# Optimization experiments

Hardware: AMD Instinct MI355X
Metric: run time of the kernel (lower is better)

The kernel has to match this reference:

```python
import jax, jax.numpy as jnp
import numpy as np
import math

B, S, D = 2048, 128, 64          # batch, seq_length, input_dim
H1, H2, OUT = 128, 128, 1        # sa_hidden, ta_hidden, output_dim


def _uniform(key, shape, stdv):
    return jax.random.uniform(key, shape, jnp.float32, -stdv, stdv)


def setup_inputs() -> dict:
    key = jax.random.key(0)
    ks = jax.random.split(key, 20)
    s1 = 1.0 / math.sqrt(H1)
    s2 = 1.0 / math.sqrt(H2)
    inp = {
        "X": jax.random.normal(ks[0], (B, S, D), jnp.float32),
        # SpatialLSTM params (stdv = 1/sqrt(sa_hidden))
        "sa_W": _uniform(ks[1], (D, 4 * H1), s1),
        "sa_U": _uniform(ks[2], (H1, 4 * H1), s1),
        "sa_b": _uniform(ks[3], (4 * H1,), s1),
        "sa_Wa": _uniform(ks[4], (D, D), s1),
        "sa_Ua": _uniform(ks[5], (2 * H1, D), s1),
        "sa_ba": _uniform(ks[6], (D,), s1),
        "sa_Va": _uniform(ks[7], (D, D), s1),
        # TemporalLSTM params (stdv = 1/sqrt(ta_hidden))
        "ta_Wa": _uniform(ks[8], (H1, S), s2),
        "ta_Ua": _uniform(ks[9], (H2, S), s2),
        "ta_ba": _uniform(ks[10], (S,), s2),
        "ta_Va": _uniform(ks[11], (S, S), s2),
        "ta_W": _uniform(ks[12], (H1, 4 * H2), s2),
        "ta_U": _uniform(ks[13], (H2, 4 * H2), s2),
        "ta_b": _uniform(ks[14], (4 * H2,), s2),
        "ta_Wy": _uniform(ks[15], (OUT, 4 * H2), s2),
        "fc_w": _uniform(ks[16], (OUT, H2), s2),
        "fc_b": _uniform(ks[17], (OUT,), s2),
    }
    return inp


def _sta_forward(X, sa_W, sa_U, sa_b, sa_Wa, sa_Ua, sa_ba, sa_Va,
                 ta_Wa, ta_Ua, ta_ba, ta_Va, ta_W, ta_U, ta_b, ta_Wy,
                 fc_w, fc_b):
    x = X[:, :, :D]                       # [B,S,D]
    y0 = X[:, 0, D - 1:].reshape(-1, OUT)  # y[:,0,:] -> [B,OUT]
    batch = x.shape[0]

    # ---- SpatialLSTM: scan over time ----
    def sa_step(carry, x_t):
        h, c = carry
        a = jnp.tanh(x_t @ sa_Wa + jnp.concatenate([h, c], axis=1) @ sa_Ua + sa_ba) @ sa_Va
        alpha = jax.nn.softmax(a, axis=1)            # [B,D]
        xw = alpha * x_t
        gates = xw @ sa_W + h @ sa_U + sa_b          # [B,4H1]
        i = jax.nn.sigmoid(gates[:, :H1])
        f = jax.nn.sigmoid(gates[:, H1:2 * H1])
        g = jnp.tanh(gates[:, 2 * H1:3 * H1])
        o = jax.nn.sigmoid(gates[:, 3 * H1:])
        c = f * c + i * g
        h = o * jnp.tanh(c)
        return (h, c), (h, alpha)

    h0 = jnp.zeros((batch, H1), X.dtype)
    c0 = jnp.zeros((batch, H1), X.dtype)
    _, (hs, alphas) = jax.lax.scan(sa_step, (h0, c0), jnp.swapaxes(x, 0, 1))
    H = jnp.swapaxes(hs, 0, 1)  # [B,S,H1]

    # ---- TemporalLSTM: scan over time, attending over the full H ----
    # note: s_t in the original stays zero for all t, so its s_t @ Ua term is 0.
    def ta_step(carry, h_t):
        lh, lc, y_prev = carry
        beta = jax.nn.softmax(jnp.tanh(h_t @ ta_Wa + ta_ba) @ ta_Va, axis=1)  # [B,S]
        h_att = jnp.einsum('bs,bsd->bd', beta, H)     # weighted sum over time
        gates = h_att @ ta_W + lh @ ta_U + y_prev @ ta_Wy + ta_b
        i = jax.nn.sigmoid(gates[:, :H2])
        f = jax.nn.sigmoid(gates[:, H2:2 * H2])
        g = jnp.tanh(gates[:, 2 * H2:3 * H2])
        o = jax.nn.sigmoid(gates[:, 3 * H2:])
        lc = f * lc + i * g
        lh = o * jnp.tanh(lc)
        y = lh @ fc_w.T + fc_b
        return (lh, lc, y), beta

    lh0 = jnp.zeros((batch, H2), X.dtype)
    lc0 = jnp.zeros((batch, H2), X.dtype)
    (_, _, y_pred), betas = jax.lax.scan(ta_step, (lh0, lc0, y0), jnp.swapaxes(H, 0, 1))
    return y_pred, alphas, betas  # alphas: [S,B,D], betas: [S,B,S]


def reference(X, sa_W, sa_U, sa_b, sa_Wa, sa_Ua, sa_ba, sa_Va,
              ta_Wa, ta_Ua, ta_ba, ta_Va, ta_W, ta_U, ta_b, ta_Wy,
              fc_w, fc_b):
    return _sta_forward(X, sa_W, sa_U, sa_b, sa_Wa, sa_Ua, sa_ba, sa_Va,
                        ta_Wa, ta_Ua, ta_ba, ta_Va, ta_W, ta_U, ta_b, ta_Wy,
                        fc_w, fc_b)
```

## Files before the change

kernel.cpp:

```cpp
#include <hip/hip_runtime.h>


#define BB 2048
#define SS 128
#define DD 64
#define HH 128
#define NG 512
#define M  8
#define NT 512

#define A_OFF    ((size_t)BB)
#define BETA_OFF ((size_t)BB + (size_t)SS*BB*DD)
#define H_BYTES  ((size_t)BB*SS*HH*4)
#define G0_BYTES ((size_t)BB*SS*NG*4)

#define B1G_ELEMS (192*512)
#define B1A_ELEMS (320*64)
#define BVA_ELEMS (64*64)
#define B3_ELEMS  (256*512)
#define BW_ELEMS  (128*128)
#define GH_OFF 0
#define GL_OFF (B1G_ELEMS)
#define AH_OFF (2*B1G_ELEMS)
#define AL_OFF (2*B1G_ELEMS + B1A_ELEMS)
// ... 27 lines not shown
__device__ __forceinline__ float wmax64(float v){
#pragma unroll
  for (int m = 32; m; m >>= 1) v = fmaxf(v, __shfl_xor(v, m, 64));
  return v;
}
__device__ __forceinline__ float wsum64(float v){
#pragma unroll
  for (int m = 32; m; m >>= 1) v += __shfl_xor(v, m, 64);
  return v;
}

__global__ __launch_bounds__(256) void repack_kernel(
    const float* __restrict__ saW, const float* __restrict__ saU,
    const float* __restrict__ saWa, const float* __restrict__ saUa,
    const float* __restrict__ saVa,
    const float* __restrict__ taU, const float* __restrict__ taW,
    const float* __restrict__ taWa, const float* __restrict__ taVa,
    unsigned short* __restrict__ F)
{
  int id = blockIdx.x*256 + threadIdx.x;
  if (id < B1G_ELEMS){
    int k = id >> 9, n = id & 511;
    float v = (k < 128) ? saU[(size_t)k*NG + n] : saW[(size_t)(k-128)*NG + n];
    int kk = k >> 5, kw = k & 31, nt = n >> 4, nc = n & 15;
    int lane = ((kw >> 3) << 4) | nc, j = kw & 7;
    size_t off = ((size_t)(nt*6 + kk)*64 + lane)*8 + j;
    unsigned short hi = bf16rne(v);
    F[GH_OFF + off] = hi; F[GL_OFF + off] = bf16rne(v - bfval(hi));
  }
  if (id < B1A_ELEMS){
    int k = id >> 6, n = id & 63;
    float v = (k < 256) ? saUa[(size_t)k*DD + n] : saWa[(size_t)(k-256)*DD + n];
    int kt = k >> 5, kw = k & 31, nt = n >> 4, nc = n & 15;
    int lane = ((kw >> 3) << 4) | nc, j = kw & 7;
    size_t off = ((size_t)(nt*10 + kt)*64 + lane)*8 + j;
    unsigned short hi = bf16rne(v);
    F[AH_OFF + off] = hi; F[AL_OFF + off] = bf16rne(v - bfval(hi));
  }
  if (id < BVA_ELEMS){
    int k = id >> 6, n = id & 63;
    float v = saVa[(size_t)k*DD + n];
    int kt = k >> 5, kw = k & 31, nt = n >> 4, nc = n & 15;
    int lane = ((kw >> 3) << 4) | nc, j = kw & 7;
    size_t off = ((size_t)(nt*2 + kt)*64 + lane)*8 + j;
    unsigned short hi = bf16rne(v);
    F[VH_OFF + off] = hi; F[VL_OFF + off] = bf16rne(v - bfval(hi));
  }
  if (id < B3_ELEMS){
    int k = id >> 9, n = id & 511;
    float v = (k < HH) ? taU[(size_t)k*NG + n] : taW[(size_t)(k-HH)*NG + n];
    int kt = k >> 5, kw = k & 31, nt = n >> 4, nc = n & 15;
    int lane = ((kw >> 3) << 4) | nc, j = kw & 7;
    size_t off = ((size_t)(nt*8 + kt)*64 + lane)*8 + j;
    unsigned short hi = bf16rne(v);
    F[B3H_OFF + off] = hi; F[B3L_OFF + off] = bf16rne(v - bfval(hi));
  }
  if (id < BW_ELEMS){
    int k = id >> 7, n = id & 127;
    int kt = k >> 5, kw = k & 31, nt = n >> 4, nc = n & 15;
    int lane = ((kw >> 3) << 4) | nc, j = kw & 7;
    size_t off = ((size_t)(nt*4 + kt)*64 + lane)*8 + j;
    F[RW_OFF + off] = bf16rne(taWa[(size_t)k*SS + n]);
    F[RV_OFF + off] = bf16rne(taVa[(size_t)k*SS + n]);
  }
}

struct P1 {
  uint4 afh[12*64];
  uint4 afl[12*64];
  uint4 aah[2*64];
  uint4 aal[2*64];
  uint4 awh[2560];
  uint4 awl[2560];
  uint4 vh[512];
  uint4 vl[512];
  float xx[M][DD];
  float cc[M][HH];
  float red[2][M][64];
  float g[M][NG];
  float sbias[NG];
};
struct P2S { float A[32][HH]; float tmp[32][SS]; float bp[32][SS]; };

__global__ __launch_bounds__(NT, 2) __attribute__((amdgpu_waves_per_eu(2, 2)))
void mf_ph1_kernel(
    const float* __restrict__ X,   const float* __restrict__ sab,
    const float* __restrict__ saba,
    const unsigned short* __restrict__ Fr,
    float* __restrict__ out, float* __restrict__ Hws)
{
  __shared__ P1 sm;
  const int tid = threadIdx.x;
  const int b0  = blockIdx.x * M;
  const int w   = tid >> 6, l = tid & 63;

  {
    uint4 z4 = make_uint4(0,0,0,0);
    for (int i = tid; i < 12*64; i += NT){ sm.afh[i] = z4; sm.afl[i] = z4; }
    if (tid < 2*64){ sm.aah[tid] = z4; sm.aal[tid] = z4; }
    for (int i = tid; i < M*HH; i += NT) ((float*)sm.cc)[i] = 0.f;
    sm.sbias[tid] = sab[tid];
    const uint4* sh = (const uint4*)(Fr + AH_OFF);
    const uint4* sl = (const uint4*)(Fr + AL_OFF);
    for (int i = tid; i < 2560; i += NT){ sm.awh[i] = sh[i]; sm.awl[i] = sl[i]; }
    sm.vh[tid] = ((const uint4*)(Fr + VH_OFF))[tid];
    sm.vl[tid] = ((const uint4*)(Fr + VL_OFF))[tid];
  }
  __syncthreads();
  if (tid < 128){
    int r = tid >> 4, d0 = (tid & 15)*4;
    float4 v = *(const float4*)(X + (size_t)(b0+r)*SS*DD + d0);
    *(float4*)&sm.xx[r][d0] = v;
    unsigned short* AFH = (unsigned short*)sm.afh;
    unsigned short* AFL = (unsigned short*)sm.afl;
    int kt = 8 + (d0 >> 5), lane = (((d0 & 31) >> 3) << 4) | r, jj0 = d0 & 7;
    float vv[4] = {v.x, v.y, v.z, v.w};
#pragma unroll
    for (int p = 0; p < 4; ++p){
      unsigned short h_ = bf16rne(vv[p]);
      AFH[(kt*64 + lane)*8 + jj0 + p] = h_;
      AFL[(kt*64 + lane)*8 + jj0 + p] = bf16rne(vv[p] - bfval(h_));
    }
  }
  __syncthreads();

  for (int t = 0; t < SS; ++t){
    f32x4 accg[4];
    {
      f32x4 zf = {0.f,0.f,0.f,0.f};
#pragma unroll
      for (int n4 = 0; n4 < 4; ++n4) accg[n4] = zf;
    }
    {
      const int nt = w & 3, kh = w >> 2;
      f32x4 a0 = {0.f,0.f,0.f,0.f}, a1 = {0.f,0.f,0.f,0.f};
#pragma unroll
      for (int q = 0; q < 5; ++q){
        const int kt = kh*5 + q;
        bf16x8 ah = as_bf(sm.afh[kt*64 + l]);
        bf16x8 av = as_bf(sm.afl[kt*64 + l]);
        bf16x8 bh = as_bf(sm.awh[(nt*10 + kt)*64 + l]);
        bf16x8 bl = as_bf(sm.awl[(nt*10 + kt)*64 + l]);
        if (q & 1){
          a1 = __builtin_amdgcn_mfma_f32_16x16x32_bf16(ah, bh, a1, 0, 0, 0);
          a1 = __builtin_amdgcn_mfma_f32_16x16x32_bf16(av, bh, a1, 0, 0, 0);
          a1 = __builtin_amdgcn_mfma_f32_16x16x32_bf16(ah, bl, a1, 0, 0, 0);
        } else {
          a0 = __builtin_amdgcn_mfma_f32_16x16x32_bf16(ah, bh, a0, 0, 0, 0);
          a0 = __builtin_amdgcn_mfma_f32_16x16x32_bf16(av, bh, a0, 0, 0, 0);
          a0 = __builtin_amdgcn_mfma_f32_16x16x32_bf16(ah, bl, a0, 0, 0, 0);
        }
      }
      f32x4 acc = a0 + a1;
      const int row0 = (l >> 4)*4, c0 = l & 15;
      if (row0 < 8){
#pragma unroll
        for (int jj = 0; jj < 4; ++jj)
          sm.red[kh][row0+jj][nt*16 + c0] = acc[jj];
      }
      const uint4* GH = (const uint4*)(Fr + GH_OFF);
      const uint4* GL = (const uint4*)(Fr + GL_OFF);
#pragma unroll
      for (int kk = 0; kk < 4; ++kk){
        bf16x8 ah = as_bf(sm.afh[kk*64 + l]);
        bf16x8 av = as_bf(sm.afl[kk*64 + l]);
#pragma unroll
        for (int n4 = 0; n4 < 4; ++n4){
          const int ntg = w*4 + n4;
          bf16x8 bh = as_bf(GH[(ntg*6 + kk)*64 + l]);
          bf16x8 bl = as_bf(GL[(ntg*6 + kk)*64 + l]);
          accg[n4] = __builtin_amdgcn_mfma_f32_16x16x32_bf16(ah, bh, accg[n4], 0, 0, 0);
          accg[n4] = __builtin_amdgcn_mfma_f32_16x16x32_bf16(av, bh, accg[n4], 0, 0, 0);
          accg[n4] = __builtin_amdgcn_mfma_f32_16x16x32_bf16(ah, bl, accg[n4], 0, 0, 0);
        }
      }
    }
    __syncthreads();

    {
      const int r = w, col = l;
      float s = sm.red[0][r][col] + sm.red[1][r][col] + saba[col];
      float av = tanhx(s);
      unsigned short h_ = bf16rne(av);
      int kt = col >> 5, lane = (((col & 31) >> 3) << 4) | r, jj = col & 7;
      ((unsigned short*)sm.aah)[(kt*64 + lane)*8 + jj] = h_;
      ((unsigned short*)sm.aal)[(kt*64 + lane)*8 + jj] = bf16rne(av - bfval(h_));
    }
    __syncthreads();

    {
      const int nt = w & 3, kt = w >> 2;
      f32x4 acc = {0.f,0.f,0.f,0.f};
      bf16x8 ah = as_bf(sm.aah[kt*64 + l]);
      bf16x8 av = as_bf(sm.aal[kt*64 + l]);
      bf16x8 bh = as_bf(sm.vh[(nt*2 + kt)*64 + l]);
      bf16x8 bl = as_bf(sm.vl[(nt*2 + kt)*64 + l]);
      acc = __builtin_amdgcn_mfma_f32_16x16x32_bf16(ah, bh, acc, 0, 0, 0);
      acc = __builtin_amdgcn_mfma_f32_16x16x32_bf16(av, bh, acc, 0, 0, 0);
      acc = __builtin_amdgcn_mfma_f32_16x16x32_bf16(ah, bl, acc, 0, 0, 0);
      const int row0 = (l >> 4)*4, c0 = l & 15;
      if (row0 < 8){
#pragma unroll
        for (int jj = 0; jj < 4; ++jj)
          sm.red[kt][row0+jj][nt*16 + c0] = acc[jj];
      }
    }
    __syncthreads();

    {
      const int r = w, col = l;
      float s = sm.red[0][r][col] + sm.red[1][r][col];
      float mm = wmax64(s);
      float e  = __expf(s - mm);
      float alv = e * (1.0f / wsum64(e));
      out[A_OFF + (size_t)t*BB*DD + (size_t)(b0+r)*DD + col] = alv;
      float xwv = alv * sm.xx[r][col];
      unsigned short h_ = bf16rne(xwv);
      int kt = 10 + (col >> 5), lane = (((col & 31) >> 3) << 4) | r, jj = col & 7;
      ((unsigned short*)sm.afh)[(kt*64 + lane)*8 + jj] = h_;
      ((unsigned short*)sm.afl)[(kt*64 + lane)*8 + jj] = bf16rne(xwv - bfval(h_));
    }
    __syncthreads();

    float4 pf;
    const bool dox = (tid < 128) && (t + 1 < SS);
    if (dox){
      int r = tid >> 4, d0 = (tid & 15)*4;
      pf = *(const float4*)(X + (size_t)(b0+r)*SS*DD + (size_t)(t+1)*DD + d0);
    }
    {
      const uint4* GH = (const uint4*)(Fr + GH_OFF);
      const uint4* GL = (const uint4*)(Fr + GL_OFF);
#pragma unroll
      for (int kk = 4; kk < 6; ++kk){
        const int afi = kk + 6;
        bf16x8 ah = as_bf(sm.afh[afi*64 + l]);
        bf16x8 av = as_bf(sm.afl[afi*64 + l]);
#pragma unroll
        for (int n4 = 0; n4 < 4; ++n4){
          const int ntg = w*4 + n4;
          bf16x8 bh = as_bf(GH[(ntg*6 + kk)*64 + l]);
          bf16x8 bl = as_bf(GL[(ntg*6 + kk)*64 + l]);
          accg[n4] = __builtin_amdgcn_mfma_f32_16x16x32_bf16(ah, bh, accg[n4], 0, 0, 0);
          accg[n4] = __builtin_amdgcn_mfma_f32_16x16x32_bf16(av, bh, accg[n4], 0, 0, 0);
          accg[n4] = __builtin_amdgcn_mfma_f32_16x16x32_bf16(ah, bl, accg[n4], 0, 0, 0);
        }
      }
      const int row0 = (l >> 4)*4, c0 = l & 15;
      if (row0 < 8){
#pragma unroll
        for (int n4 = 0; n4 < 4; ++n4){
          int col = w*64 + n4*16 + c0;
          float b = sm.sbias[col];
#pragma unroll
          for (int jj = 0; jj < 4; ++jj)
            sm.g[row0+jj][col] = accg[n4][jj] + b;
        }
      }
    }
    __syncthreads();

    {
      unsigned short* AFH = (unsigned short*)sm.afh;
      unsigned short* AFL = (unsigned short*)sm.afl;
#pragma unroll
      for (int h2 = 0; h2 < 2; ++h2){
        int idx = h2*NT + tid;
        int r = idx >> 7, j = idx & 127;
        float iv = sigf (sm.g[r][j]);
        float fv = sigf (sm.g[r][j + 128]);
        float gv = tanhx(sm.g[r][j + 256]);
        float ov = sigf (sm.g[r][j + 384]);
        float cn = fv * sm.cc[r][j] + iv * gv;
        float hn = ov * tanhx(cn);
        sm.cc[r][j] = cn;
        Hws[(size_t)(b0+r)*SS*HH + (size_t)t*HH + j] = hn;
        int lane = (((j & 31) >> 3) << 4) | r, jj = j & 7;
        int ktH = j >> 5, ktC = 4 + (j >> 5);
        unsigned short hh_ = bf16rne(hn);
        unsigned short ch_ = bf16rne(cn);
        AFH[(ktH*64 + lane)*8 + jj] = hh_;
        AFL[(ktH*64 + lane)*8 + jj] = bf16rne(hn - bfval(hh_));
        AFH[(ktC*64 + lane)*8 + jj] = ch_;
        AFL[(ktC*64 + lane)*8 + jj] = bf16rne(cn - bfval(ch_));
      }
      if (dox){
        int r = tid >> 4, d0 = (tid & 15)*4;
        *(float4*)&sm.xx[r][d0] = pf;
        int kt = 8 + (d0 >> 5), lane = (((d0 & 31) >> 3) << 4) | r, jj0 = d0 & 7;
        float vv[4] = {pf.x, pf.y, pf.z, pf.w};
#pragma unroll
        for (int p = 0; p < 4; ++p){
          unsigned short h_ = bf16rne(vv[p]);
          AFH[(kt*64 + lane)*8 + jj0 + p] = h_;
          AFL[(kt*64 + lane)*8 + jj0 + p] = bf16rne(vv[p] - bfval(h_));
        }
      }
    }
    __syncthreads();
  }
}

struct PH2G {
  union { unsigned short S[128][136]; float SG[128][68]; } u1;
  unsigned short S2[128][136];
  uint4 fA[8][4][64];
  uint4 fB[8][4][64];
  float bias[SS];
};

__global__ __launch_bounds__(NT, 2) void ph2g_kernel(
    const float* __restrict__ taba, const unsigned short* __restrict__ Fr,
    const float* __restrict__ tab,
    float* __restrict__ out, float* __restrict__ Hws, float* __restrict__ G0)
{
  __shared__ PH2G sm;
  const int tid = threadIdx.x;
  const int b   = blockIdx.x;
  const int w   = tid >> 6, l = tid & 63;
  const int g   = l >> 4, c0 = l & 15;
  const float* Hb = Hws + (size_t)b * SS * HH;

  if (tid < SS) sm.bias[tid] = taba[tid];
  {
    const float4* src = (const float4*)Hb;
#pragma unroll
    for (int i = 0; i < 8; ++i){
      int fidx = i*NT + tid;
      float4 v = src[fidx];
      int e0 = fidx*4, row = e0 >> 7, col = e0 & 127;
      sm.u1.S[row][col+0] = bf16rne(v.x);
      sm.u1.S[row][col+1] = bf16rne(v.y);
      sm.u1.S[row][col+2] = bf16rne(v.z);
      sm.u1.S[row][col+3] = bf16rne(v.w);
    }
  }
  __syncthreads();

#pragma unroll
  for (int i = 0; i < 4; ++i){
    int slot = i*NT + tid;
    int mt = slot >> 8, kt = (slot >> 6) & 3, ll = slot & 63;
    int row = mt*16 + (ll & 15), k0 = kt*32 + (ll >> 4)*8;
    ((uint4*)sm.fA)[slot] = *(const uint4*)&sm.u1.S[row][k0];
  }
#pragma unroll
  for (int i = 0; i < 4; ++i){
    int slot = i*NT + tid;
    int nt = slot >> 8, kt = (slot >> 6) & 3, ll = slot & 63;
    int col = nt*16 + (ll & 15), s0 = kt*32 + (ll >> 4)*8;
    unsigned u[4];
#pragma unroll
    for (int p = 0; p < 4; ++p)
      u[p] = (unsigned)sm.u1.S[s0+2*p][col] | ((unsigned)sm.u1.S[s0+2*p+1][col] << 16);
    ((uint4*)sm.fB)[slot] = make_uint4(u[0], u[1], u[2], u[3]);
  }
  __syncthreads();

  f32x4 acc[8];
  f32x4 zero4 = {0.f, 0.f, 0.f, 0.f};

#pragma unroll
  for (int nt = 0; nt < 8; ++nt) acc[nt] = zero4;
  {
    const uint4* BW = (const uint4*)(Fr + RW_OFF);
#pragma unroll
    for (int kt = 0; kt < 4; ++kt){
      bf16x8 a = as_bf(sm.fA[w][kt][l]);
#pragma unroll
      for (int nt = 0; nt < 8; ++nt){
        bf16x8 bv = as_bf(BW[(nt*4 + kt)*64 + l]);
        acc[nt] = __builtin_amdgcn_mfma_f32_16x16x32_bf16(a, bv, acc[nt], 0, 0, 0);
      }
    }
  }
#pragma unroll
  for (int nt = 0; nt < 8; ++nt){
    int col = nt*16 + c0;
    float bv = sm.bias[col];
#pragma unroll
    for (int j = 0; j < 4; ++j)
      sm.u1.S[w*16 + g*4 + j][col] = bf16rne(tanhx(acc[nt][j] + bv));
  }
  __syncthreads();

#pragma unroll
  for (int i = 0; i < 4; ++i){
    int slot = i*NT + tid;
    int mt = slot >> 8, kt = (slot >> 6) & 3, ll = slot & 63;
    int row = mt*16 + (ll & 15), k0 = kt*32 + (ll >> 4)*8;
    ((uint4*)sm.fA)[slot] = *(const uint4*)&sm.u1.S[row][k0];
  }
  __syncthreads();

#pragma unroll
  for (int nt = 0; nt < 8; ++nt) acc[nt] = zero4;
  {
    const uint4* BV = (const uint4*)(Fr + RV_OFF);
#pragma unroll
    for (int kt = 0; kt < 4; ++kt){
      bf16x8 a = as_bf(sm.fA[w][kt][l]);
#pragma unroll
      for (int nt = 0; nt < 8; ++nt){
        bf16x8 bv = as_bf(BV[(nt*4 + kt)*64 + l]);
        acc[nt] = __builtin_amdgcn_mfma_f32_16x16x32_bf16(a, bv, acc[nt], 0, 0, 0);
      }
    }
  }

#pragma unroll
  for (int j = 0; j < 4; ++j){
    float m = acc[0][j];
#pragma unroll
    for (int nt = 1; nt < 8; ++nt) m = fmaxf(m, acc[nt][j]);
#pragma unroll
    for (int ms = 1; ms < 16; ms <<= 1) m = fmaxf(m, __shfl_xor(m, ms, 64));
    float e[8], s = 0.f;
#pragma unroll
    for (int nt = 0; nt < 8; ++nt){ e[nt] = __expf(acc[nt][j] - m); s += e[nt]; }
#pragma unroll
    for (int ms = 1; ms < 16; ms <<= 1) s += __shfl_xor(s, ms, 64);
    float inv = 1.0f / s;
    int row = w*16 + g*4 + j;
    size_t bo = BETA_OFF + (size_t)row*BB*SS + (size_t)b*SS;
#pragma unroll
    for (int nt = 0; nt < 8; ++nt){
      float bv = e[nt] * inv;
      out[bo + nt*16 + c0] = bv;
      sm.u1.S[row][nt*16 + c0] = bf16rne(bv);
    }
  }
  __syncthreads();

#pragma unroll
  for (int i = 0; i < 4; ++i){
    int slot = i*NT + tid;
    int mt = slot >> 8, kt = (slot >> 6) & 3, ll = slot & 63;
    int row = mt*16 + (ll & 15), k0 = kt*32 + (ll >> 4)*8;
    ((uint4*)sm.fA)[slot] = *(const uint4*)&sm.u1.S[row][k0];
  }
  __syncthreads();

#pragma unroll
  for (int nt = 0; nt < 8; ++nt) acc[nt] = zero4;
#pragma unroll
  for (int kt = 0; kt < 4; ++kt){
    bf16x8 a = as_bf(sm.fA[w][kt][l]);
#pragma unroll
    for (int nt = 0; nt < 8; ++nt){
      bf16x8 bv = as_bf(sm.fB[nt][kt][l]);
      acc[nt] = __builtin_amdgcn_mfma_f32_16x16x32_bf16(a, bv, acc[nt], 0, 0, 0);
    }
  }
#pragma unroll
  for (int nt = 0; nt < 8; ++nt){
#pragma unroll
    for (int j = 0; j < 4; ++j){
      int row = w*16 + g*4 + j, col = nt*16 + c0;
      float v = acc[nt][j];
      unsigned short h_ = bf16rne(v);
      sm.u1.S[row][col] = h_;
      sm.S2[row][col]   = bf16rne(v - bfval(h_));
    }
  }
  __syncthreads();

#pragma unroll
  for (int i = 0; i < 4; ++i){
    int slot = i*NT + tid;
    int mt = slot >> 8, kt = (slot >> 6) & 3, ll = slot & 63;
    int row = mt*16 + (ll & 15), k0 = kt*32 + (ll >> 4)*8;
    ((uint4*)sm.fA)[slot] = *(const uint4*)&sm.u1.S[row][k0];
    ((uint4*)sm.fB)[slot] = *(const uint4*)&sm.S2[row][k0];
  }
  __syncthreads();

  const uint4* BH = (const uint4*)(Fr + B3H_OFF);
  const uint4* BL = (const uint4*)(Fr + B3L_OFF);
  const size_t r0 = (size_t)b * SS;
#pragma unroll
  for (int p = 0; p < 8; ++p){
    f32x4 acc2[4];
#pragma unroll
    for (int q = 0; q < 4; ++q) acc2[q] = zero4;
#pragma unroll
    for (int q = 0; q < 4; ++q){
      const int ntg = p*4 + q;
#pragma unroll
      for (int kt = 0; kt < 4; ++kt){
        bf16x8 ah = as_bf(sm.fA[w][kt][l]);
        bf16x8 av = as_bf(sm.fB[w][kt][l]);
        bf16x8 bh = as_bf(BH[(ntg*8 + 4 + kt)*64 + l]);
        bf16x8 bl = as_bf(BL[(ntg*8 + 4 + kt)*64 + l]);
        acc2[q] = __builtin_amdgcn_mfma_f32_16x16x32_bf16(ah, bh, acc2[q], 0, 0, 0);
        acc2[q] = __builtin_amdgcn_mfma_f32_16x16x32_bf16(av, bh, acc2[q], 0, 0, 0);
        acc2[q] = __builtin_amdgcn_mfma_f32_16x16x32_bf16(ah, bl, acc2[q], 0, 0, 0);
      }
    }
#pragma unroll
    for (int q = 0; q < 4; ++q){
      float tb = tab[p*64 + q*16 + c0];
#pragma unroll
      for (int j = 0; j < 4; ++j)
        sm.u1.SG[w*16 + g*4 + j][q*16 + c0] = acc2[q][j] + tb;
    }
    __syncthreads();
#pragma unroll
    for (int it = 0; it < 4; ++it){
      int flat = it*NT + tid;
      int row = flat >> 4, cq = flat & 15;
      *(float4*)(G0 + (r0 + row)*NG + p*64 + cq*4) = *(const float4*)&sm.u1.SG[row][cq*4];
    }
    __syncthreads();
  }
}

struct PH2SM {
  union {
    struct { uint4 fA[8][4][64]; uint4 fB[8][4][64]; } f;
    float HO[128][132];
  } u;
  unsigned short S[128][136];
  float bias[SS];
};

__global__ __launch_bounds__(NT, 2) void ph2_kernel(
    const float* __restrict__ taba, const unsigned short* __restrict__ Fr,
    float* __restrict__ out, float* __restrict__ Hws)
{
  __shared__ PH2SM sm;
  const int tid = threadIdx.x;
  const int b   = blockIdx.x;
  const int w   = tid >> 6, l = tid & 63;
  const int g   = l >> 4, c0 = l & 15;
  float* Hb = Hws + (size_t)b * SS * HH;

  if (tid < SS) sm.bias[tid] = taba[tid];
  {
    const float4* src = (const float4*)Hb;
#pragma unroll
    for (int i = 0; i < 8; ++i){
      int fidx = i*NT + tid;
      float4 v = src[fidx];
      int e0 = fidx*4, row = e0 >> 7, col = e0 & 127;
      sm.S[row][col+0] = bf16rne(v.x);
      sm.S[row][col+1] = bf16rne(v.y);
      sm.S[row][col+2] = bf16rne(v.z);
      sm.S[row][col+3] = bf16rne(v.w);
    }
  }
  __syncthreads();

#pragma unroll
  for (int i = 0; i < 4; ++i){
    int slot = i*NT + tid;
    int mt = slot >> 8, kt = (slot >> 6) & 3, ll = slot & 63;
    int row = mt*16 + (ll & 15), k0 = kt*32 + (ll >> 4)*8;
    ((uint4*)sm.u.f.fA)[slot] = *(const uint4*)&sm.S[row][k0];
  }
#pragma unroll
  for (int i = 0; i < 4; ++i){
    int slot = i*NT + tid;
    int nt = slot >> 8, kt = (slot >> 6) & 3, ll = slot & 63;
    int col = nt*16 + (ll & 15), s0 = kt*32 + (ll >> 4)*8;
    unsigned u[4];
#pragma unroll
    for (int p = 0; p < 4; ++p)
      u[p] = (unsigned)sm.S[s0+2*p][col] | ((unsigned)sm.S[s0+2*p+1][col] << 16);
    ((uint4*)sm.u.f.fB)[slot] = make_uint4(u[0], u[1], u[2], u[3]);
  }
  __syncthreads();

  f32x4 acc[8];
  f32x4 zero4 = {0.f, 0.f, 0.f, 0.f};

#pragma unroll
  for (int nt = 0; nt < 8; ++nt) acc[nt] = zero4;
  {
    const uint4* BW = (const uint4*)(Fr + RW_OFF);
#pragma unroll
    for (int kt = 0; kt < 4; ++kt){
      bf16x8 a = as_bf(sm.u.f.fA[w][kt][l]);
#pragma unroll
      for (int nt = 0; nt < 8; ++nt){
        bf16x8 bv = as_bf(BW[(nt*4 + kt)*64 + l]);
        acc[nt] = __builtin_amdgcn_mfma_f32_16x16x32_bf16(a, bv, acc[nt], 0, 0, 0);
      }
    }
  }
#pragma unroll
  for (int nt = 0; nt < 8; ++nt){
    int col = nt*16 + c0;
    float bv = sm.bias[col];
#pragma unroll
    for (int j = 0; j < 4; ++j)
      sm.S[w*16 + g*4 + j][col] = bf16rne(tanhx(acc[nt][j] + bv));
  }
  __syncthreads();

#pragma unroll
  for (int i = 0; i < 4; ++i){
    int slot = i*NT + tid;
    int mt = slot >> 8, kt = (slot >> 6) & 3, ll = slot & 63;
    int row = mt*16 + (ll & 15), k0 = kt*32 + (ll >> 4)*8;
    ((uint4*)sm.u.f.fA)[slot] = *(const uint4*)&sm.S[row][k0];
  }
  __syncthreads();

#pragma unroll
  for (int nt = 0; nt < 8; ++nt) acc[nt] = zero4;
  {
    const uint4* BV = (const uint4*)(Fr + RV_OFF);
#pragma unroll
    for (int kt = 0; kt < 4; ++kt){
      bf16x8 a = as_bf(sm.u.f.fA[w][kt][l]);
#pragma unroll
      for (int nt = 0; nt < 8; ++nt){
        bf16x8 bv = as_bf(BV[(nt*4 + kt)*64 + l]);
        acc[nt] = __builtin_amdgcn_mfma_f32_16x16x32_bf16(a, bv, acc[nt], 0, 0, 0);
      }
    }
  }

#pragma unroll
  for (int j = 0; j < 4; ++j){
    float m = acc[0][j];
#pragma unroll
    for (int nt = 1; nt < 8; ++nt) m = fmaxf(m, acc[nt][j]);
#pragma unroll
    for (int ms = 1; ms < 16; ms <<= 1) m = fmaxf(m, __shfl_xor(m, ms, 64));
    float e[8], s = 0.f;
#pragma unroll
    for (int nt = 0; nt < 8; ++nt){ e[nt] = __expf(acc[nt][j] - m); s += e[nt]; }
#pragma unroll
    for (int ms = 1; ms < 16; ms <<= 1) s += __shfl_xor(s, ms, 64);
    float inv = 1.0f / s;
    int row = w*16 + g*4 + j;
    size_t bo = BETA_OFF + (size_t)row*BB*SS + (size_t)b*SS;
#pragma unroll
    for (int nt = 0; nt < 8; ++nt){
      float bv = e[nt] * inv;
      out[bo + nt*16 + c0] = bv;
      sm.S[row][nt*16 + c0] = bf16rne(bv);
    }
  }
  __syncthreads();

#pragma unroll
  for (int i = 0; i < 4; ++i){
    int slot = i*NT + tid;
    int mt = slot >> 8, kt = (slot >> 6) & 3, ll = slot & 63;
    int row = mt*16 + (ll & 15), k0 = kt*32 + (ll >> 4)*8;
    ((uint4*)sm.u.f.fA)[slot] = *(const uint4*)&sm.S[row][k0];
  }
  __syncthreads();

#pragma unroll
  for (int nt = 0; nt < 8; ++nt) acc[nt] = zero4;
#pragma unroll
  for (int kt = 0; kt < 4; ++kt){
    bf16x8 a = as_bf(sm.u.f.fA[w][kt][l]);
#pragma unroll
    for (int nt = 0; nt < 8; ++nt){
      bf16x8 bv = as_bf(sm.u.f.fB[nt][kt][l]);
      acc[nt] = __builtin_amdgcn_mfma_f32_16x16x32_bf16(a, bv, acc[nt], 0, 0, 0);
    }
  }
  __syncthreads();

#pragma unroll
  for (int nt = 0; nt < 8; ++nt)
#pragma unroll
    for (int j = 0; j < 4; ++j)
      sm.u.HO[w*16 + g*4 + j][nt*16 + c0] = acc[nt][j];
  __syncthreads();
#pragma unroll
  for (int it = 0; it < 8; ++it){
    int flat = it*NT + tid;
    int row = flat >> 5, cq = flat & 31;
    *(float4*)(Hb + (size_t)row*HH + cq*4) = *(const float4*)&sm.u.HO[row][cq*4];
  }
}

struct P3H {
  uint4 afh[4*64];
  uint4 afl[4*64];
  float lh[M][HH];
  float lc[M][HH];
  float g[M][NG];
  float wy[NG];
  float fcv[HH];
  float yp[M];
};
union __align__(16) SMCH { P3H s; float pad[21504]; };

__global__ __launch_bounds__(NT, 2) __attribute__((amdgpu_waves_per_eu(2, 2)))
void mf_ph3h_kernel(
    const float* __restrict__ X, const unsigned short* __restrict__ Fr,
    const float* __restrict__ G0,
    const float* __restrict__ taWy,
    const float* __restrict__ fcw, const float* __restrict__ fcb,
    float* __restrict__ out)
{
  __shared__ SMCH sm;
  const int tid = threadIdx.x;
  const int b0  = blockIdx.x * M;
  const int w   = tid >> 6, l = tid & 63;
  const int row0 = (l >> 4)*4, c0 = l & 15;

  {
    uint4 z4 = make_uint4(0,0,0,0);
    if (tid < 4*64){ sm.s.afh[tid] = z4; sm.s.afl[tid] = z4; }
    for (int i = tid; i < M*HH; i += NT){
      ((float*)sm.s.lh)[i] = 0.f; ((float*)sm.s.lc)[i] = 0.f;
    }
    sm.s.wy[tid] = taWy[tid];
    if (tid < HH) sm.s.fcv[tid] = fcw[tid];
    if (tid < M)  sm.s.yp[tid] = X[(size_t)(b0+tid)*SS*DD + (DD-1)];
  }
  float g0v[16];
  if (row0 < 8){
#pragma unroll
    for (int n4 = 0; n4 < 4; ++n4)
#pragma unroll
      for (int j = 0; j < 4; ++j)
        g0v[n4*4+j] = G0[((size_t)(b0+row0+j)*SS + 0)*NG + (w*64 + n4*16 + c0)];
  }
  __syncthreads();

  for (int t = 0; t < SS; ++t){
    {
      f32x4 zero4 = {0.f,0.f,0.f,0.f};
      f32x4 acc[4];
#pragma unroll
      for (int n4 = 0; n4 < 4; ++n4) acc[n4] = zero4;
      const uint4* BH = (const uint4*)(Fr + B3H_OFF);
      const uint4* BL = (const uint4*)(Fr + B3L_OFF);
#pragma unroll
      for (int kt = 0; kt < 4; ++kt){
        bf16x8 ah = as_bf(sm.s.afh[kt*64 + l]);
        bf16x8 av = as_bf(sm.s.afl[kt*64 + l]);
#pragma unroll
        for (int n4 = 0; n4 < 4; ++n4){
          const int ntg = w*4 + n4;
          bf16x8 bh = as_bf(BH[(ntg*8 + kt)*64 + l]);
          bf16x8 bl = as_bf(BL[(ntg*8 + kt)*64 + l]);
          acc[n4] = __builtin_amdgcn_mfma_f32_16x16x32_bf16(ah, bh, acc[n4], 0, 0, 0);
          acc[n4] = __builtin_amdgcn_mfma_f32_16x16x32_bf16(av, bh, acc[n4], 0, 0, 0);
          acc[n4] = __builtin_amdgcn_mfma_f32_16x16x32_bf16(ah, bl, acc[n4], 0, 0, 0);
        }
      }
      if (row0 < 8){
#pragma unroll
        for (int n4 = 0; n4 < 4; ++n4){
          int col = w*64 + n4*16 + c0;
          float wv = sm.s.wy[col];
#pragma unroll
          for (int j = 0; j < 4; ++j)
            sm.s.g[row0+j][col] = acc[n4][j] + g0v[n4*4+j] + sm.s.yp[row0+j]*wv;
        }
      }
    }
    __syncthreads();

    float g0n[16];
    const bool dog = (t + 1 < SS) && (row0 < 8);
    if (dog){
#pragma unroll
      for (int n4 = 0; n4 < 4; ++n4)
#pragma unroll
        for (int j = 0; j < 4; ++j)
          g0n[n4*4+j] = G0[((size_t)(b0+row0+j)*SS + (t+1))*NG + (w*64 + n4*16 + c0)];
    }
    {
      unsigned short* AFH = (unsigned short*)sm.s.afh;
      unsigned short* AFL = (unsigned short*)sm.s.afl;
#pragma unroll
      for (int h2 = 0; h2 < 2; ++h2){
        int idx = h2*NT + tid;
        int r = idx >> 7, j = idx & 127;
        float iv = sigf (sm.s.g[r][j]);
        float fv = sigf (sm.s.g[r][j + 128]);
        float gv = tanhx(sm.s.g[r][j + 256]);
        float ov = sigf (sm.s.g[r][j + 384]);
        float cn = fv * sm.s.lc[r][j] + iv * gv;
        float hn = ov * tanhx(cn);
        sm.s.lc[r][j] = cn; sm.s.lh[r][j] = hn;
        int kt = j >> 5, lane = (((j & 31) >> 3) << 4) | r, jj = j & 7;
        unsigned short h_ = bf16rne(hn);
        AFH[(kt*64 + lane)*8 + jj] = h_;
        AFL[(kt*64 + lane)*8 + jj] = bf16rne(hn - bfval(h_));
      }
    }
    __syncthreads();

    {
      const int r = w, lx = l;
      float p = sm.s.lh[r][lx]*sm.s.fcv[lx] + sm.s.lh[r][lx+64]*sm.s.fcv[lx+64];
      p = wsum64(p);
      if (lx == 0) sm.s.yp[r] = p + fcb[0];
    }
    if (dog){
#pragma unroll
      for (int q = 0; q < 16; ++q) g0v[q] = g0n[q];
    }
    __syncthreads();
  }

  if (tid < M) out[b0 + tid] = sm.s.yp[tid];
}

struct P3 {
  uint4 afh[8*64];
  uint4 afl[8*64];
  float lh[M][HH];
  float lc[M][HH];
  float g[M][NG];
  float sb[NG];
  float wy[NG];
  float fcv[HH];
  float yp[M];
};
union __align__(16) SMC { P3 s; float pad[21504]; };

__global__ __launch_bounds__(NT, 2) void mf_ph3_kernel(
    const float* __restrict__ X, const float* __restrict__ Ha,
    const unsigned short* __restrict__ Fr,
    const float* __restrict__ tab, const float* __restrict__ taWy,
    const float* __restrict__ fcw, const float* __restrict__ fcb,
    float* __restrict__ out)
{
  __shared__ SMC sm;
  const int tid = threadIdx.x;
  const int b0  = blockIdx.x * M;
  const int w   = tid >> 6, l = tid & 63;

  {
    uint4 z4 = make_uint4(0,0,0,0);
    sm.s.afh[tid] = z4; sm.s.afl[tid] = z4;
    for (int i = tid; i < M*HH; i += NT){
      ((float*)sm.s.lh)[i] = 0.f; ((float*)sm.s.lc)[i] = 0.f;
    }
    sm.s.sb[tid] = tab[tid];
    sm.s.wy[tid] = taWy[tid];
    if (tid < HH) sm.s.fcv[tid] = fcw[tid];
    if (tid < M)  sm.s.yp[tid] = X[(size_t)(b0+tid)*SS*DD + (DD-1)];
  }
  __syncthreads();
  if (tid < 256){
    int r = tid >> 5, d0 = (tid & 31)*4;
    float4 v = *(const float4*)(Ha + (size_t)(b0+r)*SS*HH + d0);
    unsigned short* AFH = (unsigned short*)sm.s.afh;
    unsigned short* AFL = (unsigned short*)sm.s.afl;
    int kt = 4 + (d0 >> 5), lane = (((d0 & 31) >> 3) << 4) | r, jj0 = d0 & 7;
    float vv[4] = {v.x, v.y, v.z, v.w};
#pragma unroll
    for (int p = 0; p < 4; ++p){
      unsigned short h_ = bf16rne(vv[p]);
      AFH[(kt*64 + lane)*8 + jj0 + p] = h_;
      AFL[(kt*64 + lane)*8 + jj0 + p] = bf16rne(vv[p] - bfval(h_));
    }
  }
  __syncthreads();

  for (int t = 0; t < SS; ++t){
    float4 pf;
    const bool dop = (tid < 256) && (t + 1 < SS);
    if (dop){
      int r = tid >> 5, d0 = (tid & 31)*4;
      pf = *(const float4*)(Ha + (size_t)(b0+r)*SS*HH + (size_t)(t+1)*HH + d0);
    }
    {
      f32x4 zero4 = {0.f,0.f,0.f,0.f};
      f32x4 acc[4];
#pragma unroll
      for (int n4 = 0; n4 < 4; ++n4) acc[n4] = zero4;
      const uint4* BH = (const uint4*)(Fr + B3H_OFF);
      const uint4* BL = (const uint4*)(Fr + B3L_OFF);
#pragma unroll
      for (int kt = 0; kt < 8; ++kt){
        bf16x8 ah = as_bf(sm.s.afh[kt*64 + l]);
        bf16x8 av = as_bf(sm.s.afl[kt*64 + l]);
#pragma unroll
        for (int n4 = 0; n4 < 4; ++n4){
          const int ntg = w*4 + n4;
          bf16x8 bh = as_bf(BH[(ntg*8 + kt)*64 + l]);
          bf16x8 bl = as_bf(BL[(ntg*8 + kt)*64 + l]);
          acc[n4] = __builtin_amdgcn_mfma_f32_16x16x32_bf16(ah, bh, acc[n4], 0, 0, 0);
          acc[n4] = __builtin_amdgcn_mfma_f32_16x16x32_bf16(av, bh, acc[n4], 0, 0, 0);
          acc[n4] = __builtin_amdgcn_mfma_f32_16x16x32_bf16(ah, bl, acc[n4], 0, 0, 0);
        }
      }
      const int row0 = (l >> 4)*4;
      if (row0 < 8){
        const int colb = w*64 + (l & 15);
#pragma unroll
        for (int n4 = 0; n4 < 4; ++n4){
          int col = colb + n4*16;
          float b = sm.s.sb[col];
          float wv = sm.s.wy[col];
#pragma unroll
          for (int j = 0; j < 4; ++j)
            sm.s.g[row0+j][col] = acc[n4][j] + b + sm.s.yp[row0+j]*wv;
        }
      }
    }
    __syncthreads();

    {
      unsigned short* AFH = (unsigned short*)sm.s.afh;
      unsigned short* AFL = (unsigned short*)sm.s.afl;
#pragma unroll
      for (int h2 = 0; h2 < 2; ++h2){
        int idx = h2*NT + tid;
        int r = idx >> 7, j = idx & 127;
        float iv = sigf (sm.s.g[r][j]);
        float fv = sigf (sm.s.g[r][j + 128]);
        float gv = tanhx(sm.s.g[r][j + 256]);
        float ov = sigf (sm.s.g[r][j + 384]);
        float cn = fv * sm.s.lc[r][j] + iv * gv;
        float hn = ov * tanhx(cn);
        sm.s.lc[r][j] = cn; sm.s.lh[r][j] = hn;
        int kt = j >> 5, lane = (((j & 31) >> 3) << 4) | r, jj = j & 7;
        unsigned short h_ = bf16rne(hn);
        AFH[(kt*64 + lane)*8 + jj] = h_;
        AFL[(kt*64 + lane)*8 + jj] = bf16rne(hn - bfval(h_));
      }
    }
    __syncthreads();

    {
      const int r = w, lx = l;
      float p = sm.s.lh[r][lx]*sm.s.fcv[lx] + sm.s.lh[r][lx+64]*sm.s.fcv[lx+64];
      p = wsum64(p);
      if (lx == 0) sm.s.yp[r] = p + fcb[0];
    }
    if (dop){
      int r = tid >> 5, d0 = (tid & 31)*4;
      unsigned short* AFH = (unsigned short*)sm.s.afh;
      unsigned short* AFL = (unsigned short*)sm.s.afl;
      int kt = 4 + (d0 >> 5), lane = (((d0 & 31) >> 3) << 4) | r, jj0 = d0 & 7;
      float vv[4] = {pf.x, pf.y, pf.z, pf.w};
#pragma unroll
      for (int p = 0; p < 4; ++p){
        unsigned short h_ = bf16rne(vv[p]);
        AFH[(kt*64 + lane)*8 + jj0 + p] = h_;
        AFL[(kt*64 + lane)*8 + jj0 + p] = bf16rne(vv[p] - bfval(h_));
      }
    }
    __syncthreads();
  }

  if (tid < M) out[b0 + tid] = sm.s.yp[tid];
}

struct FSM1 {
  float x[M][DD]; float h[M][HH]; float c[M][HH];
  float a[M][DD]; float xw[M][DD]; float g[M][NG];
};
struct FP1 { FSM1 s; float red[8][512]; };
union __align__(16) FSMA { FP1 p1; P2S p2; float pad[21504]; };

__global__ __launch_bounds__(NT, 2) void fb_ph12_kernel(
    const float* __restrict__ X,
    const float* __restrict__ saW,  const float* __restrict__ saU,  const float* __restrict__ sab,
    const float* __restrict__ saWa, const float* __restrict__ saUa, const float* __restrict__ saba,
    const float* __restrict__ saVa,
    const float* __restrict__ taWa, const float* __restrict__ taba, const float* __restrict__ taVa,
    float* __restrict__ out, float* __restrict__ Hws)
{
  __shared__ FSMA sm;
  const int tid = threadIdx.x;
  const int b0  = blockIdx.x * M;
  const int w   = tid >> 6, l = tid & 63;

  for (int idx = tid; idx < M*HH; idx += NT){
    int r = idx >> 7, j = idx & 127;
    sm.p1.s.h[r][j] = 0.f; sm.p1.s.c[r][j] = 0.f;
  }
  { int r = tid >> 6, d = tid & 63;
    sm.p1.s.x[r][d] = X[(size_t)(b0+r)*SS*DD + d]; }
  __syncthreads();

  for (int t = 0; t < SS; ++t){
    {
      float pr[M];
#pragma unroll
      for (int r = 0; r < M; ++r) pr[r] = 0.f;
      { const int kb = w*8;
#pragma unroll
        for (int q = 0; q < 2; ++q){
          const int k = kb + q*4;
          const float* wp = saWa + (size_t)k*DD + l;
          float w0 = wp[0], w1 = wp[DD], w2 = wp[2*DD], w3 = wp[3*DD];
#pragma unroll
          for (int r = 0; r < M; ++r){
            float4 v = *(const float4*)&sm.p1.s.x[r][k];
            pr[r] += w0*v.x + w1*v.y + w2*v.z + w3*v.w;
          }
        }
      }
      { const int kb = w*16;
#pragma unroll
        for (int q = 0; q < 4; ++q){
          const int k = kb + q*4;
          const float* wp = saUa + (size_t)k*DD + l;
          float w0 = wp[0], w1 = wp[DD], w2 = wp[2*DD], w3 = wp[3*DD];
#pragma unroll
          for (int r = 0; r < M; ++r){
            float4 v = *(const float4*)&sm.p1.s.h[r][k];
            pr[r] += w0*v.x + w1*v.y + w2*v.z + w3*v.w;
          }
        }
      }
      { const int kb = w*16;
#pragma unroll
        for (int q = 0; q < 4; ++q){
          const int k = kb + q*4;
          const float* wp = saUa + (size_t)(HH + k)*DD + l;
          float w0 = wp[0], w1 = wp[DD], w2 = wp[2*DD], w3 = wp[3*DD];
#pragma unroll
          for (int r = 0; r < M; ++r){
            float4 v = *(const float4*)&sm.p1.s.c[r][k];
            pr[r] += w0*v.x + w1*v.y + w2*v.z + w3*v.w;
          }
        }
      }
#pragma unroll
      for (int r = 0; r < M; ++r) sm.p1.red[w][r*64 + l] = pr[r];
    }
    __syncthreads();
    {
      float s = saba[l];
#pragma unroll
      for (int u = 0; u < 8; ++u) s += sm.p1.red[u][w*64 + l];
      sm.p1.s.a[w][l] = tanhx(s);
    }
    __syncthreads();
    {
      float pr[M];
#pragma unroll
      for (int r = 0; r < M; ++r) pr[r] = 0.f;
      const int kb = w*8;
#pragma unroll
      for (int q = 0; q < 2; ++q){
        const int k = kb + q*4;
        const float* wp = saVa + (size_t)k*DD + l;
        float w0 = wp[0], w1 = wp[DD], w2 = wp[2*DD], w3 = wp[3*DD];
#pragma unroll
        for (int r = 0; r < M; ++r){
          float4 v = *(const float4*)&sm.p1.s.a[r][k];
          pr[r] += w0*v.x + w1*v.y + w2*v.z + w3*v.w;
        }
      }
#pragma unroll
      for (int r = 0; r < M; ++r) sm.p1.red[w][r*64 + l] = pr[r];
    }
    __syncthreads();
    {
      float s = 0.f;
#pragma unroll
      for (int u = 0; u < 8; ++u) s += sm.p1.red[u][w*64 + l];
      float mm = wmax64(s);
      float e  = __expf(s - mm);
      float al = e * (1.0f / wsum64(e));
      out[A_OFF + (size_t)t*BB*DD + (size_t)(b0+w)*DD + l] = al;
      sm.p1.s.xw[w][l] = al * sm.p1.s.x[w][l];
    }
    __syncthreads();
    {
      const int c0 = tid;
      float acc[M];
      const float bv = sab[c0];
#pragma unroll
      for (int r = 0; r < M; ++r) acc[r] = bv;
      for (int k = 0; k < DD; k += 4){
        const float* wp = saW + (size_t)k*NG + c0;
        float w0 = wp[0], w1 = wp[NG], w2 = wp[2*NG], w3 = wp[3*NG];
#pragma unroll
        for (int r = 0; r < M; ++r){
          float4 v = *(const float4*)&sm.p1.s.xw[r][k];
          acc[r] += w0*v.x + w1*v.y + w2*v.z + w3*v.w;
        }
      }
      for (int k = 0; k < HH; k += 4){
        const float* wp = saU + (size_t)k*NG + c0;
        float w0 = wp[0], w1 = wp[NG], w2 = wp[2*NG], w3 = wp[3*NG];
#pragma unroll
        for (int r = 0; r < M; ++r){
          float4 v = *(const float4*)&sm.p1.s.h[r][k];
          acc[r] += w0*v.x + w1*v.y + w2*v.z + w3*v.w;
        }
      }
#pragma unroll
      for (int r = 0; r < M; ++r) sm.p1.s.g[r][c0] = acc[r];
    }
    __syncthreads();
    for (int idx = tid; idx < M*HH; idx += NT){
      int r = idx >> 7, j = idx & 127;
      float iv = sigf (sm.p1.s.g[r][j]);
      float fv = sigf (sm.p1.s.g[r][j +   HH]);
      float gv = tanhx(sm.p1.s.g[r][j + 2*HH]);
      float ov = sigf (sm.p1.s.g[r][j + 3*HH]);
      float cn = fv * sm.p1.s.c[r][j] + iv * gv;
      float hn = ov * tanhx(cn);
      sm.p1.s.c[r][j] = cn; sm.p1.s.h[r][j] = hn;
      Hws[(size_t)(b0+r)*SS*HH + (size_t)t*HH + j] = hn;
    }
    if (t + 1 < SS){
      int r = tid >> 6, d = tid & 63;
      sm.p1.s.x[r][d] = X[(size_t)(b0+r)*SS*DD + (size_t)(t+1)*DD + d];
    }
// ... 219 lines not shown
```

Measured before the change: 1.432 ms.

## Write MFMA fragments directly, widen G0 tiles, fuse fc reduction into LSTM step

In the phase-2 kernel, the split hi/lo bf16 accumulator values are now written straight into the MFMA fragment layout. This drops the S2 staging buffer, one barrier and a shared-memory reshuffle pass. The G0 projection loop now runs in 4 passes of 128 columns instead of 8 passes of 64, halving the number of barrier pairs at the cost of more accumulator registers. In the temporal recurrence kernel, the fc output dot product is computed as partial wave sums inside the gate-update loop, which removes one __syncthreads per timestep; the partials are combined at the start of the next step.

```diff
diff --git a/kernel.cpp b/kernel.cpp
--- a/kernel.cpp
+++ b/kernel.cpp
@@ -353,8 +353,7 @@
 }
 
 struct PH2G {
-  union { unsigned short S[128][136]; float SG[128][68]; } u1;
-  unsigned short S2[128][136];
+  union { unsigned short S[128][136]; float SG[128][132]; } u;
   uint4 fA[8][4][64];
   uint4 fB[8][4][64];
   float bias[SS];
@@ -380,10 +379,10 @@
       int fidx = i*NT + tid;
       float4 v = src[fidx];
       int e0 = fidx*4, row = e0 >> 7, col = e0 & 127;
-      sm.u1.S[row][col+0] = bf16rne(v.x);
-      sm.u1.S[row][col+1] = bf16rne(v.y);
-      sm.u1.S[row][col+2] = bf16rne(v.z);
-      sm.u1.S[row][col+3] = bf16rne(v.w);
+      sm.u.S[row][col+0] = bf16rne(v.x);
+      sm.u.S[row][col+1] = bf16rne(v.y);
+      sm.u.S[row][col+2] = bf16rne(v.z);
+      sm.u.S[row][col+3] = bf16rne(v.w);
     }
   }
   __syncthreads();
@@ -393,7 +392,7 @@
     int slot = i*NT + tid;
     int mt = slot >> 8, kt = (slot >> 6) & 3, ll = slot & 63;
     int row = mt*16 + (ll & 15), k0 = kt*32 + (ll >> 4)*8;
-    ((uint4*)sm.fA)[slot] = *(const uint4*)&sm.u1.S[row][k0];
+    ((uint4*)sm.fA)[slot] = *(const uint4*)&sm.u.S[row][k0];
   }
 #pragma unroll
   for (int i = 0; i < 4; ++i){
@@ -403,7 +402,7 @@
     unsigned u[4];
 #pragma unroll
     for (int p = 0; p < 4; ++p)
-      u[p] = (unsigned)sm.u1.S[s0+2*p][col] | ((unsigned)sm.u1.S[s0+2*p+1][col] << 16);
+      u[p] = (unsigned)sm.u.S[s0+2*p][col] | ((unsigned)sm.u.S[s0+2*p+1][col] << 16);
     ((uint4*)sm.fB)[slot] = make_uint4(u[0], u[1], u[2], u[3]);
   }
   __syncthreads();
@@ -431,7 +430,7 @@
     float bv = sm.bias[col];
 #pragma unroll
     for (int j = 0; j < 4; ++j)
-      sm.u1.S[w*16 + g*4 + j][col] = bf16rne(tanhx(acc[nt][j] + bv));
+      sm.u.S[w*16 + g*4 + j][col] = bf16rne(tanhx(acc[nt][j] + bv));
   }
   __syncthreads();
 
@@ -440,7 +439,7 @@
     int slot = i*NT + tid;
     int mt = slot >> 8, kt = (slot >> 6) & 3, ll = slot & 63;
     int row = mt*16 + (ll & 15), k0 = kt*32 + (ll >> 4)*8;
-    ((uint4*)sm.fA)[slot] = *(const uint4*)&sm.u1.S[row][k0];
+    ((uint4*)sm.fA)[slot] = *(const uint4*)&sm.u.S[row][k0];
   }
   __syncthreads();
 
@@ -478,7 +477,7 @@
     for (int nt = 0; nt < 8; ++nt){
       float bv = e[nt] * inv;
       out[bo + nt*16 + c0] = bv;
-      sm.u1.S[row][nt*16 + c0] = bf16rne(bv);
+      sm.u.S[row][nt*16 + c0] = bf16rne(bv);
     }
   }
   __syncthreads();
@@ -488,7 +487,7 @@
     int slot = i*NT + tid;
     int mt = slot >> 8, kt = (slot >> 6) & 3, ll = slot & 63;
     int row = mt*16 + (ll & 15), k0 = kt*32 + (ll >> 4)*8;
-    ((uint4*)sm.fA)[slot] = *(const uint4*)&sm.u1.S[row][k0];
+    ((uint4*)sm.fA)[slot] = *(const uint4*)&sm.u.S[row][k0];
   }
   __syncthreads();
 
@@ -503,40 +502,39 @@
       acc[nt] = __builtin_amdgcn_mfma_f32_16x16x32_bf16(a, bv, acc[nt], 0, 0, 0);
     }
   }
-#pragma unroll
-  for (int nt = 0; nt < 8; ++nt){
-#pragma unroll
-    for (int j = 0; j < 4; ++j){
-      int row = w*16 + g*4 + j, col = nt*16 + c0;
-      float v = acc[nt][j];
-      unsigned short h_ = bf16rne(v);
-      sm.u1.S[row][col] = h_;
-      sm.S2[row][col]   = bf16rne(v - bfval(h_));
-    }
-  }
-  __syncthreads();
-
-#pragma unroll
-  for (int i = 0; i < 4; ++i){
-    int slot = i*NT + tid;
-    int mt = slot >> 8, kt = (slot >> 6) & 3, ll = slot & 63;
-    int row = mt*16 + (ll & 15), k0 = kt*32 + (ll >> 4)*8;
-    ((uint4*)sm.fA)[slot] = *(const uint4*)&sm.u1.S[row][k0];
-    ((uint4*)sm.fB)[slot] = *(const uint4*)&sm.S2[row][k0];
-  }
-  __syncthreads();
+  __syncthreads();
+
+  {
+    unsigned short* FH = (unsigned short*)sm.fA;
+    unsigned short* FL = (unsigned short*)sm.fB;
+    const int jj = c0 & 7;
+#pragma unroll
+    for (int nt = 0; nt < 8; ++nt){
+      const int kt = nt >> 1;
+      const int laneb = ((nt & 1)*2 + (c0 >> 3))*16;
+#pragma unroll
+      for (int j = 0; j < 4; ++j){
+        int lane = laneb + (g*4 + j);
+        float v = acc[nt][j];
+        unsigned short h_ = bf16rne(v);
+        size_t idxs = ((size_t)(w*4 + kt)*64 + lane)*8 + jj;
+        FH[idxs] = h_;
+        FL[idxs] = bf16rne(v - bfval(h_));
+      }
+    }
+  }
 
   const uint4* BH = (const uint4*)(Fr + B3H_OFF);
   const uint4* BL = (const uint4*)(Fr + B3L_OFF);
   const size_t r0 = (size_t)b * SS;
 #pragma unroll
-  for (int p = 0; p < 8; ++p){
-    f32x4 acc2[4];
-#pragma unroll
-    for (int q = 0; q < 4; ++q) acc2[q] = zero4;
-#pragma unroll
-    for (int q = 0; q < 4; ++q){
-      const int ntg = p*4 + q;
+  for (int p = 0; p < 4; ++p){
+    f32x4 acc2[8];
+#pragma unroll
+    for (int q = 0; q < 8; ++q) acc2[q] = zero4;
+#pragma unroll
+    for (int q = 0; q < 8; ++q){
+      const int ntg = p*8 + q;
 #pragma unroll
       for (int kt = 0; kt < 4; ++kt){
         bf16x8 ah = as_bf(sm.fA[w][kt][l]);
@@ -549,18 +547,18 @@
       }
     }
 #pragma unroll
-    for (int q = 0; q < 4; ++q){
-      float tb = tab[p*64 + q*16 + c0];
+    for (int q = 0; q < 8; ++q){
+      float tb = tab[p*128 + q*16 + c0];
 #pragma unroll
       for (int j = 0; j < 4; ++j)
-        sm.u1.SG[w*16 + g*4 + j][q*16 + c0] = acc2[q][j] + tb;
-    }
-    __syncthreads();
-#pragma unroll
-    for (int it = 0; it < 4; ++it){
+        sm.u.SG[w*16 + g*4 + j][q*16 + c0] = acc2[q][j] + tb;
+    }
+    __syncthreads();
+#pragma unroll
+    for (int it = 0; it < 8; ++it){
       int flat = it*NT + tid;
-      int row = flat >> 4, cq = flat & 15;
-      *(float4*)(G0 + (r0 + row)*NG + p*64 + cq*4) = *(const float4*)&sm.u1.SG[row][cq*4];
+      int row = flat >> 5, cq = flat & 31;
+      *(float4*)(G0 + (r0 + row)*NG + p*128 + cq*4) = *(const float4*)&sm.u.SG[row][cq*4];
     }
     __syncthreads();
   }
@@ -741,7 +739,9 @@
   float g[M][NG];
   float wy[NG];
   float fcv[HH];
-  float yp[M];
+  float red[M][2];
+  float ypinit[M];
+  float fcb0;
 };
 union __align__(16) SMCH { P3H s; float pad[21504]; };
 
@@ -767,7 +767,8 @@
     }
     sm.s.wy[tid] = taWy[tid];
     if (tid < HH) sm.s.fcv[tid] = fcw[tid];
-    if (tid < M)  sm.s.yp[tid] = X[(size_t)(b0+tid)*SS*DD + (DD-1)];
+    if (tid < M)  sm.s.ypinit[tid] = X[(size_t)(b0+tid)*SS*DD + (DD-1)];
+    if (tid == 0) sm.s.fcb0 = fcb[0];
   }
   float g0v[16];
   if (row0 < 8){
@@ -781,6 +782,15 @@
 
   for (int t = 0; t < SS; ++t){
     {
+      float ypr[4];
+      if (row0 < 8){
+#pragma unroll
+        for (int j = 0; j < 4; ++j){
+          int r = row0 + j;
+          ypr[j] = (t == 0) ? sm.s.ypinit[r]
+                            : (sm.s.red[r][0] + sm.s.red[r][1] + sm.s.fcb0);
+        }
+      }
       f32x4 zero4 = {0.f,0.f,0.f,0.f};
       f32x4 acc[4];
 #pragma unroll
@@ -808,7 +818,7 @@
           float wv = sm.s.wy[col];
 #pragma unroll
           for (int j = 0; j < 4; ++j)
-            sm.s.g[row0+j][col] = acc[n4][j] + g0v[n4*4+j] + sm.s.yp[row0+j]*wv;
+            sm.s.g[row0+j][col] = acc[n4][j] + g0v[n4*4+j] + ypr[j]*wv;
         }
       }
     }
@@ -841,15 +851,10 @@
         unsigned short h_ = bf16rne(hn);
         AFH[(kt*64 + lane)*8 + jj] = h_;
         AFL[(kt*64 + lane)*8 + jj] = bf16rne(hn - bfval(h_));
-      }
-    }
-    __syncthreads();
-
-    {
-      const int r = w, lx = l;
-      float p = sm.s.lh[r][lx]*sm.s.fcv[lx] + sm.s.lh[r][lx+64]*sm.s.fcv[lx+64];
-      p = wsum64(p);
-      if (lx == 0) sm.s.yp[r] = p + fcb[0];
+        float ps = hn * sm.s.fcv[j];
+        ps = wsum64(ps);
+        if (l == 0) sm.s.red[r][w & 1] = ps;
+      }
     }
     if (dog){
 #pragma unroll
@@ -858,7 +863,7 @@
     __syncthreads();
   }
 
-  if (tid < M) out[b0 + tid] = sm.s.yp[tid];
+  if (tid < M) out[b0 + tid] = sm.s.red[tid][0] + sm.s.red[tid][1] + sm.s.fcb0;
 }
 
 struct P3 {
```

Result: faster. 1.383 ms (-3.4%).
